# Optimization experiments

Measured on AMD Instinct MI355X. Metric: run time of the kernel, lower is better.

Reference implementation:

```python
import jax, jax.numpy as jnp
import numpy as np

EMBED_DIM = 1024
NUM_HEADS = 16
KEY_SIZE = 1024
VALUE_SIZE = 1024
N, L = 4, 2048


def setup_inputs() -> dict:
    key = jax.random.key(0)
    ks = jax.random.split(key, 8)
    s = lambda fan_in: 1.0 / np.sqrt(fan_in)
    return {
        "x": jax.random.normal(ks[0], (N, L, EMBED_DIM), dtype=jnp.float32),
        # nn.Linear weights stored as (out, in); we apply x @ W.T
        "W_q": jax.random.uniform(ks[1], (KEY_SIZE, EMBED_DIM), jnp.float32, -s(EMBED_DIM), s(EMBED_DIM)),
        "W_k": jax.random.uniform(ks[2], (KEY_SIZE, EMBED_DIM), jnp.float32, -s(EMBED_DIM), s(EMBED_DIM)),
        "W_v": jax.random.uniform(ks[3], (VALUE_SIZE, EMBED_DIM), jnp.float32, -s(EMBED_DIM), s(EMBED_DIM)),
        "W_qp": jax.random.uniform(ks[4], (KEY_SIZE, KEY_SIZE), jnp.float32, -s(KEY_SIZE), s(KEY_SIZE)),
        "W_kp": jax.random.uniform(ks[5], (KEY_SIZE, KEY_SIZE), jnp.float32, -s(KEY_SIZE), s(KEY_SIZE)),
        "W_vp": jax.random.uniform(ks[6], (VALUE_SIZE, VALUE_SIZE), jnp.float32, -s(VALUE_SIZE), s(VALUE_SIZE)),
        "W_out": jax.random.uniform(ks[7], (EMBED_DIM, VALUE_SIZE), jnp.float32, -s(VALUE_SIZE), s(VALUE_SIZE)),
    }


def reference(x, W_q, W_k, W_v, W_qp, W_kp, W_vp, W_out):
    H = NUM_HEADS
    q = (x @ W_q.T) @ W_qp.T   # (N, L, key_size)
    k = (x @ W_k.T) @ W_kp.T   # (N, L, key_size)
    v = (x @ W_v.T) @ W_vp.T   # (N, L, value_size)
    n, l, vs = v.shape
    dq = q.shape[-1] // H
    dv = vs // H
    q = q.reshape(n, l, H, dq).transpose(0, 2, 1, 3)  # (N, H, L, dq)
    k = k.reshape(n, l, H, dq).transpose(0, 2, 1, 3)
    v = v.reshape(n, l, H, dv).transpose(0, 2, 1, 3)
    att = jnp.einsum("nhid,nhjd->nhij", q, k) / jnp.sqrt(jnp.float32(dq))
    att = jax.nn.softmax(att, axis=-1)
    out = jnp.einsum("nhij,nhjd->nhid", att, v)       # (N, H, L, dv)
    out = out.transpose(0, 2, 1, 3).reshape(n, l, vs)
    return out @ W_out.T
```

## Files before the change

### kernel.cpp

```cpp
#include <hip/hip_runtime.h>
#include <cstddef>
#include <cstdint>

#define EMBED 1024
#define NH    16
#define DQ    64
#define NB    4
#define LSEQ  2048
#define MROWS (NB * LSEQ)

typedef __bf16 bf16x8 __attribute__((ext_vector_type(8)));
typedef float  f32x4  __attribute__((ext_vector_type(4)));

__device__ __forceinline__ unsigned short f2bf(float f) {
    return (unsigned short)((__float_as_uint(f) + 0x8000u) >> 16);
}

__device__ __forceinline__ unsigned pack2(float a, float b) {
    unsigned ua = __float_as_uint(a) + 0x8000u;
    unsigned ub = __float_as_uint(b) + 0x8000u;
    return __builtin_amdgcn_perm(ub, ua, 0x07060302u);
}

__device__ __forceinline__ uint2 pack4(float a, float b, float c, float d) {
    return make_uint2(pack2(a, b), pack2(c, d));
}

__device__ __forceinline__ unsigned pack2t(float a, float b) {
    return __builtin_amdgcn_perm(__float_as_uint(b), __float_as_uint(a), 0x07060302u);
}

__device__ __forceinline__ uint2 pack4t(float a, float b, float c, float d) {
    return make_uint2(pack2t(a, b), pack2t(c, d));
}

__device__ __forceinline__ void async_cp16(const void* g, void* l) {
    __builtin_amdgcn_global_load_lds((const __attribute__((address_space(1))) unsigned int*)g,
                                     (__attribute__((address_space(3))) unsigned int*)l,
                                     16, 0, 0);
}

struct CvtJobs {
    const float* src[8];
    unsigned short* dst[8];
    int n[8];
};

__global__ __launch_bounds__(256) void cvt_bf16(CvtJobs j) {
    int job = blockIdx.y;
    const float* s = j.src[job];
    unsigned short* d = j.dst[job];
    int n4 = j.n[job] >> 2;
    int stride = gridDim.x * blockDim.x;
    for (int i = blockIdx.x * blockDim.x + threadIdx.x; i < n4; i += stride) {
        float4 f = ((const float4*)s)[i];
        ((uint2*)d)[i] = pack4(f.x, f.y, f.z, f.w);
    }
}

struct TransJobs {
    const float* src[3];
    unsigned short* dst[3];
};

__global__ __launch_bounds__(256) void transpose_cvt(TransJobs tj) {
    __shared__ unsigned short Ts[64][68];
    const float* src = tj.src[blockIdx.z];
    unsigned short* dst = tj.dst[blockIdx.z];
    const int tid = threadIdx.x;
    const int r0 = blockIdx.y * 64;
    const int c0 = blockIdx.x * 64;

    {
        int col4 = tid & 15;
        int rb   = tid >> 4;
#pragma unroll
        for (int it = 0; it < 4; it++) {
            int r = rb + it * 16;
            float4 f = *(const float4*)(src + (size_t)(r0 + r) * 1024 + c0 + col4 * 4);
            *(uint2*)&Ts[r][col4 * 4] = pack4(f.x, f.y, f.z, f.w);
        }
    }
    __syncthreads();

    {
        int oc = tid >> 2;
        int seg = tid & 3;
        __attribute__((aligned(16))) unsigned short tmp[16];
#pragma unroll
        for (int e = 0; e < 16; e++) tmp[e] = Ts[seg * 16 + e][oc];
        unsigned short* out = dst + (size_t)(c0 + oc) * 1024 + r0 + seg * 16;
        *(uint4*)(out)     = *(const uint4*)&tmp[0];
        *(uint4*)(out + 8) = *(const uint4*)&tmp[8];
    }
}

struct BGemmArgs {
    const unsigned short* A[3];
    const unsigned short* B[3];
    void* C[3];
    int mode[3];
    float scl[3];
};

__global__ __launch_bounds__(256) void gemm_bf16nt(BGemmArgs p, int M, int N, int K) {
    __shared__ __align__(16) unsigned short SMEM[2 * 128 * 64];
    unsigned short* As = SMEM;
    unsigned short* Bs = SMEM + 128 * 64;

    const int tid  = threadIdx.x;
    const int wave = tid >> 6;
    const int lane = tid & 63;
    const int m16  = lane & 15;
    const int kq   = lane >> 4;
    const int bm = blockIdx.y * 128;
    const int bn = blockIdx.x * 128;
    const int z  = blockIdx.z;
    const unsigned short* A = p.A[z];
    const unsigned short* B = p.B[z];

    f32x4 acc[4][4];
#pragma unroll
    for (int i = 0; i < 4; i++)
#pragma unroll
        for (int j = 0; j < 4; j++) acc[i][j] = f32x4{0.f, 0.f, 0.f, 0.f};

    const int wr = (wave >> 1) * 64;
    const int wc = (wave & 1) * 64;

    for (int k0 = 0; k0 < K; k0 += 64) {
#pragma unroll
        for (int it = 0; it < 4; it++) {
            int c = tid + it * 256;
            int r = c >> 3;
            int kc = (c & 7) ^ (r & 7);
            async_cp16(A + (size_t)(bm + r) * K + k0 + kc * 8,
                       &As[(it * 256 + wave * 64) * 8]);
            async_cp16(B + (size_t)(bn + r) * K + k0 + kc * 8,
                       &Bs[(it * 256 + wave * 64) * 8]);
        }
        __syncthreads();

#pragma unroll
        for (int s = 0; s < 2; s++) {
            bf16x8 af[4], bfr[4];
#pragma unroll
            for (int i = 0; i < 4; i++) {
                int ra = wr + i * 16 + m16;
                af[i] = *reinterpret_cast<const bf16x8*>(
                    &As[ra * 64 + (((s * 4 + kq) ^ (ra & 7)) * 8)]);
                int rb = wc + i * 16 + m16;
                bfr[i] = *reinterpret_cast<const bf16x8*>(
                    &Bs[rb * 64 + (((s * 4 + kq) ^ (rb & 7)) * 8)]);
            }
#pragma unroll
            for (int i = 0; i < 4; i++)
#pragma unroll
                for (int j = 0; j < 4; j++)
                    acc[i][j] = __builtin_amdgcn_mfma_f32_16x16x32_bf16(af[i], bfr[j], acc[i][j], 0, 0, 0);
        }
        __syncthreads();
    }

    const int mode = p.mode[z];
    const float scl = p.scl[z];
    if (mode == 0) {
        unsigned short* Cb = (unsigned short*)p.C[z];
#pragma unroll
        for (int i = 0; i < 4; i++)
#pragma unroll
            for (int j = 0; j < 4; j++) {
                int row = bm + wr + i * 16 + kq * 4;
                int col = bn + wc + j * 16 + m16;
#pragma unroll
                for (int q = 0; q < 4; q++)
                    Cb[(size_t)(row + q) * N + col] = f2bf(acc[i][j][q] * scl);
            }
    } else if (mode == 1) {
        float* Cf = (float*)p.C[z];
#pragma unroll
        for (int i = 0; i < 4; i++)
#pragma unroll
            for (int j = 0; j < 4; j++) {
                int row = bm + wr + i * 16 + kq * 4;
                int col = bn + wc + j * 16 + m16;
#pragma unroll
                for (int q = 0; q < 4; q++)
                    Cf[(size_t)(row + q) * N + col] = acc[i][j][q];
            }
    } else {
        unsigned short* Tt = SMEM;
#pragma unroll
        for (int i = 0; i < 4; i++)
#pragma unroll
            for (int j = 0; j < 4; j++) {
                int c = wc + j * 16 + m16;
                int u = (wr >> 2) + i * 4 + kq;
                int us = (u + 2 * c) & 31;
                *reinterpret_cast<uint2*>(&Tt[c * 128 + us * 4]) =
                    pack4(acc[i][j][0], acc[i][j][1], acc[i][j][2], acc[i][j][3]);
            }
        __syncthreads();
        unsigned short* Ct = (unsigned short*)p.C[z];
        int r8 = tid & 15;
        int cb = tid >> 4;
#pragma unroll
        for (int pass = 0; pass < 8; pass++) {
            int c  = pass * 16 + cb;
            int u0 = r8 * 2;
            int us = (u0 + 2 * c) & 31;
            uint4 val = *reinterpret_cast<const uint4*>(&Tt[c * 128 + us * 4]);
            *reinterpret_cast<uint4*>(&Ct[(size_t)(bn + c) * M + bm + r8 * 8]) = val;
        }
    }
}

__global__ __launch_bounds__(256, 3)
void flash_bf16(const unsigned short* __restrict__ qb,
                const unsigned short* __restrict__ kb,
                const unsigned short* __restrict__ vtb,
                unsigned short* __restrict__ ao) {
    __shared__ __align__(16) unsigned short Ks[2][64 * 64];
    __shared__ __align__(16) unsigned short Vt[2][64 * 64];
    __shared__ __align__(16) unsigned short Pt[4][32 * 40];

    const int tid  = threadIdx.x;
    const int wave = tid >> 6;
    const int lane = tid & 63;
    const int m16  = lane & 15;
    const int kq   = lane >> 4;

    const int flat = blockIdx.y * (LSEQ / 128) + blockIdx.x;
    const int swz  = (flat & 7) * 128 + (flat >> 3);
    const int bh   = swz >> 4;
    const int nn   = bh >> 4;
    const int h    = bh & 15;
    const int q0   = (swz & 15) * 128;

    const uint4 ones_u = make_uint4(0x3F803F80u, 0x3F803F80u, 0x3F803F80u, 0x3F803F80u);
    const bf16x8 av_ones = __builtin_bit_cast(bf16x8, ones_u);

    const unsigned short* kptr  = kb + (size_t)(nn * LSEQ) * EMBED + h * DQ;
    const unsigned short* vtptr = vtb + (size_t)(h * DQ) * MROWS + nn * LSEQ;

    auto stage = [&](int buf, const unsigned short* kp, const unsigned short* vp) {
#pragma unroll
        for (int it = 0; it < 2; it++) {
            int c = tid + it * 256;
            int r = c >> 3;
            int kc = (c & 7) ^ (r & 7);
            async_cp16(kp + (size_t)r * EMBED + kc * 8,
                       &Ks[buf][(it * 256 + wave * 64) * 8]);
            async_cp16(vp + (size_t)r * MROWS + kc * 8,
                       &Vt[buf][(it * 256 + wave * 64) * 8]);
        }
    };

    stage(0, kptr, vtptr);
    kptr  += 64 * EMBED;
    vtptr += 64;

    bf16x8 qf[2][2];
#pragma unroll
    for (int j = 0; j < 2; j++) {
        size_t tok = (size_t)(nn * LSEQ + q0 + wave * 32 + j * 16 + m16);
#pragma unroll
        for (int s = 0; s < 2; s++)
            qf[j][s] = *reinterpret_cast<const bf16x8*>(
                &qb[tok * EMBED + h * DQ + s * 32 + kq * 8]);
    }

    f32x4 o[4][2];
    f32x4 o4[2];
#pragma unroll
    for (int j = 0; j < 2; j++) {
        o4[j] = f32x4{0.f, 0.f, 0.f, 0.f};
#pragma unroll
        for (int mt = 0; mt < 4; mt++) o[mt][j] = f32x4{0.f, 0.f, 0.f, 0.f};
    }

    asm volatile("s_waitcnt vmcnt(0)" ::: "memory");
    __builtin_amdgcn_s_barrier();
    asm volatile("" ::: "memory");

    const int NT = LSEQ / 64;
    for (int kt = 0; kt < NT; kt++) {
        const int cur = kt & 1;
        if (kt + 1 < NT) {
            stage(cur ^ 1, kptr, vtptr);
            kptr  += 64 * EMBED;
            vtptr += 64;
        }

        f32x4 st[4][2];
#pragma unroll
        for (int i = 0; i < 4; i++)
#pragma unroll
            for (int j = 0; j < 2; j++) st[i][j] = f32x4{0.f, 0.f, 0.f, 0.f};

#pragma unroll
        for (int s = 0; s < 2; s++) {
            bf16x8 ak[4];
#pragma unroll
            for (int i = 0; i < 4; i++) {
                int key = i * 16 + m16;
                ak[i] = *reinterpret_cast<const bf16x8*>(
                    &Ks[cur][key * 64 + (((s * 4 + kq) ^ (m16 & 7)) * 8)]);
            }
#pragma unroll
            for (int i = 0; i < 4; i++)
#pragma unroll
                for (int j = 0; j < 2; j++)
                    st[i][j] = __builtin_amdgcn_mfma_f32_16x16x32_bf16(ak[i], qf[j][s], st[i][j], 0, 0, 0);
        }

#pragma unroll
        for (int i = 0; i < 4; i++)
#pragma unroll
            for (int j = 0; j < 2; j++)
#pragma unroll
                for (int q = 0; q < 4; q++)
                    st[i][j][q] = __builtin_amdgcn_exp2f(st[i][j][q]);

#pragma unroll
        for (int s = 0; s < 2; s++) {
#pragma unroll
            for (int i2 = 0; i2 < 2; i2++) {
                int i = s * 2 + i2;
#pragma unroll
                for (int j = 0; j < 2; j++)
                    *reinterpret_cast<uint2*>(
                        &Pt[wave][(j * 16 + m16) * 40 + i2 * 16 + kq * 4]) =
                        pack4t(st[i][j][0], st[i][j][1], st[i][j][2], st[i][j][3]);
            }
            bf16x8 av[4], bp[2];
#pragma unroll
            for (int mt = 0; mt < 4; mt++) {
                int d = mt * 16 + m16;
                av[mt] = *reinterpret_cast<const bf16x8*>(
                    &Vt[cur][d * 64 + (((s * 4 + kq) ^ (m16 & 7)) * 8)]);
            }
#pragma unroll
            for (int j = 0; j < 2; j++)
                bp[j] = *reinterpret_cast<const bf16x8*>(
                    &Pt[wave][(j * 16 + m16) * 40 + kq * 8]);
#pragma unroll
            for (int mt = 0; mt < 4; mt++)
#pragma unroll
                for (int j = 0; j < 2; j++)
                    o[mt][j] = __builtin_amdgcn_mfma_f32_16x16x32_bf16(av[mt], bp[j], o[mt][j], 0, 0, 0);
#pragma unroll
            for (int j = 0; j < 2; j++)
                o4[j] = __builtin_amdgcn_mfma_f32_16x16x32_bf16(av_ones, bp[j], o4[j], 0, 0, 0);
        }

        asm volatile("s_waitcnt vmcnt(0) lgkmcnt(0)" ::: "memory");
        __builtin_amdgcn_s_barrier();
        asm volatile("" ::: "memory");
    }

#pragma unroll
    for (int j = 0; j < 2; j++) {
        float inv = 1.f / o4[j][0];
        size_t tok = (size_t)(nn * LSEQ + q0 + wave * 32 + j * 16 + m16);
#pragma unroll
        for (int mt = 0; mt < 4; mt++) {
            *reinterpret_cast<uint2*>(&ao[tok * EMBED + h * DQ + mt * 16 + kq * 4]) =
                pack4(o[mt][j][0] * inv, o[mt][j][1] * inv, o[mt][j][2] * inv, o[mt][j][3] * inv);
        }
    }
}

extern "C" void kernel_launch(void* const* d_in, const int* in_sizes, int n_in,
                              void* d_out, int out_size, void* d_ws, size_t ws_size,
                              hipStream_t stream) {
    (void)in_sizes; (void)n_in; (void)out_size; (void)ws_size;
    const float* x     = (const float*)d_in[0];
    const float* W_q   = (const float*)d_in[1];
    const float* W_k   = (const float*)d_in[2];
    const float* W_v   = (const float*)d_in[3];
    const float* W_qp  = (const float*)d_in[4];
    const float* W_kp  = (const float*)d_in[5];
    const float* W_vp  = (const float*)d_in[6];
    const float* W_out = (const float*)d_in[7];

    unsigned short* ws16 = (unsigned short*)d_ws;
    const size_t SZX = (size_t)MROWS * EMBED;
    const size_t SZW = (size_t)EMBED * EMBED;

    unsigned short* xb    = ws16;
    unsigned short* wqpb  = xb + SZX;
    unsigned short* wkpb  = wqpb + SZW;
    unsigned short* wvpb  = wkpb + SZW;
    unsigned short* woutb = wvpb + SZW;
    unsigned short* wqT   = woutb + SZW;
    unsigned short* wkT   = wqT + SZW;
    unsigned short* wvT   = wkT + SZW;
    unsigned short* weq   = wvT + SZW;
    unsigned short* wek   = weq + SZW;
    unsigned short* wev   = wek + SZW;
    unsigned short* qbuf  = wev + SZW;
    unsigned short* kbuf  = qbuf + SZX;
    unsigned short* vtbuf = kbuf + SZX;
    unsigned short* ao    = vtbuf + SZX;

    CvtJobs cj;
    cj.src[0] = x;     cj.dst[0] = xb;    cj.n[0] = (int)SZX;
    cj.src[1] = W_qp;  cj.dst[1] = wqpb;  cj.n[1] = (int)SZW;
    cj.src[2] = W_kp;  cj.dst[2] = wkpb;  cj.n[2] = (int)SZW;
    cj.src[3] = W_vp;  cj.dst[3] = wvpb;  cj.n[3] = (int)SZW;
    cj.src[4] = W_out; cj.dst[4] = woutb; cj.n[4] = (int)SZW;
    cvt_bf16<<<dim3(512, 5), 256, 0, stream>>>(cj);

    TransJobs tj;
    tj.src[0] = W_q; tj.src[1] = W_k; tj.src[2] = W_v;
    tj.dst[0] = wqT; tj.dst[1] = wkT; tj.dst[2] = wvT;
    transpose_cvt<<<dim3(16, 16, 3), 256, 0, stream>>>(tj);

    BGemmArgs fz;
    fz.A[0] = wqpb; fz.A[1] = wkpb; fz.A[2] = wvpb;
    fz.B[0] = wqT;  fz.B[1] = wkT;  fz.B[2] = wvT;
    fz.C[0] = weq;  fz.C[1] = wek;  fz.C[2] = wev;
    fz.mode[0] = 0; fz.mode[1] = 0; fz.mode[2] = 0;
    fz.scl[0] = 1.f; fz.scl[1] = 1.f; fz.scl[2] = 1.f;
    gemm_bf16nt<<<dim3(8, 8, 3), 256, 0, stream>>>(fz, EMBED, EMBED, EMBED);

    BGemmArgs pj;
    pj.A[0] = xb;   pj.A[1] = xb;   pj.A[2] = xb;
    pj.B[0] = weq;  pj.B[1] = wek;  pj.B[2] = wev;
    pj.C[0] = qbuf; pj.C[1] = kbuf; pj.C[2] = vtbuf;
    pj.mode[0] = 0; pj.mode[1] = 0; pj.mode[2] = 2;
    pj.scl[0] = 0.18033688f; pj.scl[1] = 1.f; pj.scl[2] = 1.f;
    gemm_bf16nt<<<dim3(8, 64, 3), 256, 0, stream>>>(pj, MROWS, EMBED, EMBED);

    flash_bf16<<<dim3(LSEQ / 128, NB * NH), 256, 0, stream>>>(qbuf, kbuf, vtbuf, ao);

    BGemmArgs og;
    og.A[0] = ao;    og.A[1] = ao;    og.A[2] = ao;
    og.C[0] = d_out; og.C[1] = d_out; og.C[2] = d_out;
    og.B[0] = woutb; og.B[1] = woutb; og.B[2] = woutb;
    og.mode[0] = 1; og.mode[1] = 1; og.mode[2] = 1;
    og.scl[0] = 1.f; og.scl[1] = 1.f; og.scl[2] = 1.f;
    gemm_bf16nt<<<dim3(8, 64, 1), 256, 0, stream>>>(og, MROWS, EMBED, EMBED);
}
```

Measured before the change: 325.9 us.

## Keep softmax probabilities in registers for PV MFMA, add GEMM tile swizzle

The flash kernel no longer round-trips the exponentiated scores through per-wave LDS. It packs them directly into bf16x4 operands and uses the 16x16x16 MFMA, whose B layout matches the QK^T accumulator layout, reading V with 4-element loads. This removes LDS writes and reads and frees LDS, so occupancy is raised to 4 waves per SIMD. It also adds s_setprio around MFMA bursts, skips the last barrier, and swizzles GEMM workgroup order for L2 locality. The trade-off is twice as many smaller MFMA instructions and narrower V loads.

```diff
diff --git a/kernel.cpp b/kernel.cpp
--- a/kernel.cpp
+++ b/kernel.cpp
@@ -10,6 +10,7 @@
 #define MROWS (NB * LSEQ)
 
 typedef __bf16 bf16x8 __attribute__((ext_vector_type(8)));
+typedef __bf16 bf16x4 __attribute__((ext_vector_type(4)));
 typedef float  f32x4  __attribute__((ext_vector_type(4)));
 
 __device__ __forceinline__ unsigned short f2bf(float f) {
@@ -28,10 +29,6 @@
 
 __device__ __forceinline__ unsigned pack2t(float a, float b) {
     return __builtin_amdgcn_perm(__float_as_uint(b), __float_as_uint(a), 0x07060302u);
-}
-
-__device__ __forceinline__ uint2 pack4t(float a, float b, float c, float d) {
-    return make_uint2(pack2t(a, b), pack2t(c, d));
 }
 
 __device__ __forceinline__ void async_cp16(const void* g, void* l) {
@@ -113,8 +110,12 @@
     const int lane = tid & 63;
     const int m16  = lane & 15;
     const int kq   = lane >> 4;
-    const int bm = blockIdx.y * 128;
-    const int bn = blockIdx.x * 128;
+
+    const int nwg  = gridDim.x * gridDim.y;
+    const int flat = blockIdx.y * gridDim.x + blockIdx.x;
+    const int swz  = (flat & 7) * (nwg >> 3) + (flat >> 3);
+    const int bm = (swz / gridDim.x) * 128;
+    const int bn = (swz % gridDim.x) * 128;
     const int z  = blockIdx.z;
     const unsigned short* A = p.A[z];
     const unsigned short* B = p.B[z];
@@ -215,14 +216,13 @@
     }
 }
 
-__global__ __launch_bounds__(256, 3)
+__global__ __launch_bounds__(256, 4)
 void flash_bf16(const unsigned short* __restrict__ qb,
                 const unsigned short* __restrict__ kb,
                 const unsigned short* __restrict__ vtb,
                 unsigned short* __restrict__ ao) {
     __shared__ __align__(16) unsigned short Ks[2][64 * 64];
     __shared__ __align__(16) unsigned short Vt[2][64 * 64];
-    __shared__ __align__(16) unsigned short Pt[4][32 * 40];
 
     const int tid  = threadIdx.x;
     const int wave = tid >> 6;
@@ -237,28 +237,28 @@
     const int h    = bh & 15;
     const int q0   = (swz & 15) * 128;
 
-    const uint4 ones_u = make_uint4(0x3F803F80u, 0x3F803F80u, 0x3F803F80u, 0x3F803F80u);
-    const bf16x8 av_ones = __builtin_bit_cast(bf16x8, ones_u);
+    const uint2 ones_u = make_uint2(0x3F803F80u, 0x3F803F80u);
+    const bf16x4 ones4 = __builtin_bit_cast(bf16x4, ones_u);
 
     const unsigned short* kptr  = kb + (size_t)(nn * LSEQ) * EMBED + h * DQ;
     const unsigned short* vtptr = vtb + (size_t)(h * DQ) * MROWS + nn * LSEQ;
 
-    auto stage = [&](int buf, const unsigned short* kp, const unsigned short* vp) {
+    auto stage = [&](int buf) {
 #pragma unroll
         for (int it = 0; it < 2; it++) {
             int c = tid + it * 256;
             int r = c >> 3;
             int kc = (c & 7) ^ (r & 7);
-            async_cp16(kp + (size_t)r * EMBED + kc * 8,
+            async_cp16(kptr + (size_t)r * EMBED + kc * 8,
                        &Ks[buf][(it * 256 + wave * 64) * 8]);
-            async_cp16(vp + (size_t)r * MROWS + kc * 8,
+            async_cp16(vtptr + (size_t)r * MROWS + kc * 8,
                        &Vt[buf][(it * 256 + wave * 64) * 8]);
         }
+        kptr  += 64 * EMBED;
+        vtptr += 64;
     };
 
-    stage(0, kptr, vtptr);
-    kptr  += 64 * EMBED;
-    vtptr += 64;
+    stage(0);
 
     bf16x8 qf[2][2];
 #pragma unroll
@@ -286,11 +286,7 @@
     const int NT = LSEQ / 64;
     for (int kt = 0; kt < NT; kt++) {
         const int cur = kt & 1;
-        if (kt + 1 < NT) {
-            stage(cur ^ 1, kptr, vtptr);
-            kptr  += 64 * EMBED;
-            vtptr += 64;
-        }
+        if (kt + 1 < NT) stage(cur ^ 1);
 
         f32x4 st[4][2];
 #pragma unroll
@@ -307,56 +303,54 @@
                 ak[i] = *reinterpret_cast<const bf16x8*>(
                     &Ks[cur][key * 64 + (((s * 4 + kq) ^ (m16 & 7)) * 8)]);
             }
+            __builtin_amdgcn_s_setprio(1);
 #pragma unroll
             for (int i = 0; i < 4; i++)
 #pragma unroll
                 for (int j = 0; j < 2; j++)
                     st[i][j] = __builtin_amdgcn_mfma_f32_16x16x32_bf16(ak[i], qf[j][s], st[i][j], 0, 0, 0);
-        }
-
+            __builtin_amdgcn_s_setprio(0);
+        }
+
+        bf16x4 pb[4][2];
 #pragma unroll
         for (int i = 0; i < 4; i++)
 #pragma unroll
-            for (int j = 0; j < 2; j++)
+            for (int j = 0; j < 2; j++) {
 #pragma unroll
                 for (int q = 0; q < 4; q++)
                     st[i][j][q] = __builtin_amdgcn_exp2f(st[i][j][q]);
-
-#pragma unroll
-        for (int s = 0; s < 2; s++) {
-#pragma unroll
-            for (int i2 = 0; i2 < 2; i2++) {
-                int i = s * 2 + i2;
-#pragma unroll
-                for (int j = 0; j < 2; j++)
-                    *reinterpret_cast<uint2*>(
-                        &Pt[wave][(j * 16 + m16) * 40 + i2 * 16 + kq * 4]) =
-                        pack4t(st[i][j][0], st[i][j][1], st[i][j][2], st[i][j][3]);
-            }
-            bf16x8 av[4], bp[2];
+                uint2 u = make_uint2(pack2t(st[i][j][0], st[i][j][1]),
+                                     pack2t(st[i][j][2], st[i][j][3]));
+                pb[i][j] = __builtin_bit_cast(bf16x4, u);
+            }
+
+#pragma unroll
+        for (int i = 0; i < 4; i++) {
+            bf16x4 av4[4];
 #pragma unroll
             for (int mt = 0; mt < 4; mt++) {
                 int d = mt * 16 + m16;
-                av[mt] = *reinterpret_cast<const bf16x8*>(
-                    &Vt[cur][d * 64 + (((s * 4 + kq) ^ (m16 & 7)) * 8)]);
-            }
+                av4[mt] = *reinterpret_cast<const bf16x4*>(
+                    &Vt[cur][d * 64 + (((2 * i + (kq >> 1)) ^ (d & 7)) * 8) + (kq & 1) * 4]);
+            }
+            __builtin_amdgcn_s_setprio(1);
+#pragma unroll
+            for (int mt = 0; mt < 4; mt++)
+#pragma unroll
+                for (int j = 0; j < 2; j++)
+                    o[mt][j] = __builtin_amdgcn_mfma_f32_16x16x16bf16_1k(av4[mt], pb[i][j], o[mt][j], 0, 0, 0);
 #pragma unroll
             for (int j = 0; j < 2; j++)
-                bp[j] = *reinterpret_cast<const bf16x8*>(
-                    &Pt[wave][(j * 16 + m16) * 40 + kq * 8]);
-#pragma unroll
-            for (int mt = 0; mt < 4; mt++)
-#pragma unroll
-                for (int j = 0; j < 2; j++)
-                    o[mt][j] = __builtin_amdgcn_mfma_f32_16x16x32_bf16(av[mt], bp[j], o[mt][j], 0, 0, 0);
-#pragma unroll
-            for (int j = 0; j < 2; j++)
-                o4[j] = __builtin_amdgcn_mfma_f32_16x16x32_bf16(av_ones, bp[j], o4[j], 0, 0, 0);
-        }
-
-        asm volatile("s_waitcnt vmcnt(0) lgkmcnt(0)" ::: "memory");
-        __builtin_amdgcn_s_barrier();
-        asm volatile("" ::: "memory");
+                o4[j] = __builtin_amdgcn_mfma_f32_16x16x16bf16_1k(ones4, pb[i][j], o4[j], 0, 0, 0);
+            __builtin_amdgcn_s_setprio(0);
+        }
+
+        if (kt + 1 < NT) {
+            asm volatile("s_waitcnt vmcnt(0)" ::: "memory");
+            __builtin_amdgcn_s_barrier();
+            asm volatile("" ::: "memory");
+        }
     }
 
 #pragma unroll
@@ -437,8 +431,8 @@
 
     BGemmArgs og;
     og.A[0] = ao;    og.A[1] = ao;    og.A[2] = ao;
+    og.B[0] = woutb; og.B[1] = woutb; og.B[2] = woutb;
     og.C[0] = d_out; og.C[1] = d_out; og.C[2] = d_out;
-    og.B[0] = woutb; og.B[1] = woutb; og.B[2] = woutb;
     og.mode[0] = 1; og.mode[1] = 1; og.mode[2] = 1;
     og.scl[0] = 1.f; og.scl[1] = 1.f; og.scl[2] = 1.f;
     gemm_bf16nt<<<dim3(8, 64, 1), 256, 0, stream>>>(og, MROWS, EMBED, EMBED);
```

New measurement: 305.8 us. 1.07x faster.
